# Kernel tuning notes

Measured on AMD Instinct MI355X. Metric: run time of the kernel, lower is better.

Reference implementation:

```python
import jax, jax.numpy as jnp
import numpy as np

EMB = 1024
NH = 16
HS = EMB // NH  # 64


def setup_inputs() -> dict:
    key = jax.random.key(0)
    k_x, k_wqkv, k_bqkv, k_wo, k_bo = jax.random.split(key, 5)
    x = jax.random.normal(k_x, (4, 2048, EMB), dtype=jnp.float32)
    s = 1.0 / np.sqrt(EMB)
    # torch nn.Linear weight is [out, in]; store as [in, out] for x @ W
    w_qkv = jax.random.uniform(k_wqkv, (EMB, 3 * EMB), dtype=jnp.float32, minval=-s, maxval=s)
    b_qkv = jax.random.uniform(k_bqkv, (3 * EMB,), dtype=jnp.float32, minval=-s, maxval=s)
    w_out = jax.random.uniform(k_wo, (EMB, EMB), dtype=jnp.float32, minval=-s, maxval=s)
    b_out = jax.random.uniform(k_bo, (EMB,), dtype=jnp.float32, minval=-s, maxval=s)
    return {"x": x, "w_qkv": w_qkv, "b_qkv": b_qkv, "w_out": w_out, "b_out": b_out}


def reference(x, w_qkv, b_qkv, w_out, b_out):
    B, T, C = x.shape
    qkv = x @ w_qkv + b_qkv  # [B, T, 3*C]
    q, k, v = jnp.split(qkv, 3, axis=-1)
    # [B, T, C] -> [B, nh, T, hs]
    def heads(t):
        return t.reshape(B, T, NH, HS).transpose(0, 2, 1, 3)
    q, k, v = heads(q), heads(k), heads(v)
    scores = jnp.einsum('bhqd,bhkd->bhqk', q, k) / jnp.sqrt(jnp.float32(HS))
    attn = jax.nn.softmax(scores, axis=-1)  # dropout=0 -> identity
    out = jnp.einsum('bhqk,bhkd->bhqd', attn, v)
    out = out.transpose(0, 2, 1, 3).reshape(B, T, NH * HS)
    return out @ w_out + b_out
```

## Files before the change

### kernel.cpp

```cpp
#include <hip/hip_runtime.h>

typedef unsigned short u16;
typedef unsigned int u32;
typedef __attribute__((ext_vector_type(8))) __bf16 bf16x8;
typedef __attribute__((ext_vector_type(4))) __bf16 bf16x4;
typedef __attribute__((ext_vector_type(4))) float f32x4;

#define GLD_AS1 const __attribute__((address_space(1))) void*
#define GLD_AS3 __attribute__((address_space(3))) void*

__device__ __forceinline__ u16 f2b(float f) {
  u32 u = __builtin_bit_cast(u32, f);
  u += 0x7fffu + ((u >> 16) & 1u);
  return (u16)(u >> 16);
}

__global__ void prep_kernel(const float* __restrict__ x, u16* __restrict__ xb,
                            const float* __restrict__ w_qkv, u16* __restrict__ wqkvt,
                            const float* __restrict__ w_out, u16* __restrict__ woutt) {
  __shared__ float tile[32][33];
  const int bid = blockIdx.x;
  const int tid = threadIdx.x;
  if (bid < 8192) {
    int i4 = (bid * 256 + tid) * 4;
    float4 v = *(const float4*)(x + i4);
    ushort4 o;
    o.x = f2b(v.x); o.y = f2b(v.y); o.z = f2b(v.z); o.w = f2b(v.w);
    *(ushort4*)(xb + i4) = o;
    return;
  }
  const float* src; u16* dst; int C, R, bx, by;
  if (bid < 11264) {
    int b = bid - 8192;
    src = w_qkv; dst = wqkvt; C = 3072; R = 1024;
    bx = b % 96; by = b / 96;
  } else {
    int b = bid - 11264;
    src = w_out; dst = woutt; C = 1024; R = 1024;
    bx = b % 32; by = b / 32;
  }
  const int c0 = bx * 32, r0 = by * 32;
  const int tx = tid & 31, ty = tid >> 5;
  #pragma unroll
  for (int i = ty; i < 32; i += 8)
    tile[i][tx] = src[(size_t)(r0 + i) * C + c0 + tx];
  __syncthreads();
  #pragma unroll
  for (int i = ty; i < 32; i += 8)
    dst[(size_t)(c0 + i) * R + r0 + tx] = f2b(tile[tx][i]);
}

template <int MODE>
__global__ __launch_bounds__(256)
void gemm_kernel(const u16* __restrict__ A, const u16* __restrict__ Bt,
                 const float* __restrict__ bias,
                 u16* __restrict__ qo, u16* __restrict__ ko, u16* __restrict__ vo,
                 float* __restrict__ outF, int N, int K) {
  __shared__ char As[16384];
  __shared__ char Bs[16384];
  const int tid = threadIdx.x;
  const int lane = tid & 63, wave = tid >> 6;

  const int m0 = blockIdx.x * 128, n0 = blockIdx.y * 128;
  const int wm = (wave >> 1) * 64, wn = (wave & 1) * 64;
  const int lr = lane & 15, lg = lane >> 4;

  const int rB = tid >> 3;
  const int cB = ((tid & 7) * 16) ^ ((rB & 7) << 4);

  const size_t strideK = (size_t)K * 2;
  const char* Ab = (const char*)(A + (size_t)m0 * K);
  const char* Bb = (const char*)(Bt + (size_t)n0 * K);

  f32x4 acc[4][4] = {};
  const int swr = (lr & 7) << 4;

  const int nk = K >> 6;
  for (int kt = 0; kt < nk; ++kt) {
    #pragma unroll
    for (int i = 0; i < 4; ++i)
      __builtin_amdgcn_global_load_lds(
          (GLD_AS1)(Ab + (size_t)(i * 32 + rB) * strideK + kt * 128 + cB),
          (GLD_AS3)(As + i * 4096 + tid * 16), 16, 0, 0);
    #pragma unroll
    for (int i = 0; i < 4; ++i)
      __builtin_amdgcn_global_load_lds(
          (GLD_AS1)(Bb + (size_t)(i * 32 + rB) * strideK + kt * 128 + cB),
          (GLD_AS3)(Bs + i * 4096 + tid * 16), 16, 0, 0);
    __syncthreads();

    bf16x8 af[4][2], bfr[4][2];
    #pragma unroll
    for (int m = 0; m < 4; ++m) {
      const int row = wm + m * 16 + lr;
      #pragma unroll
      for (int s = 0; s < 2; ++s)
        af[m][s] = *(const bf16x8*)(As + row * 128 + ((s * 64 + lg * 16) ^ swr));
    }
    #pragma unroll
    for (int n = 0; n < 4; ++n) {
      const int row = wn + n * 16 + lr;
      #pragma unroll
      for (int s = 0; s < 2; ++s)
        bfr[n][s] = *(const bf16x8*)(Bs + row * 128 + ((s * 64 + lg * 16) ^ swr));
    }
    __builtin_amdgcn_s_setprio(1);
    #pragma unroll
    for (int m = 0; m < 4; ++m)
      #pragma unroll
      for (int n = 0; n < 4; ++n) {
        acc[m][n] = __builtin_amdgcn_mfma_f32_16x16x32_bf16(af[m][0], bfr[n][0], acc[m][n], 0, 0, 0);
        acc[m][n] = __builtin_amdgcn_mfma_f32_16x16x32_bf16(af[m][1], bfr[n][1], acc[m][n], 0, 0, 0);
      }
    __builtin_amdgcn_s_setprio(0);
    __syncthreads();
  }

  if (MODE == 0) {
    const int b = m0 >> 11;
    #pragma unroll
    for (int n = 0; n < 4; ++n) {
      const int col = n0 + wn + n * 16 + lr;
      const float bv = bias[col];
      const int which = col >> 10, c = col & 1023;
      const int h = c >> 6, d = c & 63;
      #pragma unroll
      for (int m = 0; m < 4; ++m) {
        const int rowb = m0 + wm + m * 16 + lg * 4;
        const int t0 = rowb & 2047;
        if (which == 2) {
          const int tp = (t0 & ~31) | (8 * ((t0 >> 2) & 3) + 4 * ((t0 >> 4) & 1));
          ushort4 q4;
          q4.x = f2b(acc[m][n][0] + bv);
          q4.y = f2b(acc[m][n][1] + bv);
          q4.z = f2b(acc[m][n][2] + bv);
          q4.w = f2b(acc[m][n][3] + bv);
          *(ushort4*)&vo[((size_t)(b * 16 + h) * 64 + d) * 2048 + tp] = q4;
        } else {
          u16* dst = (which == 0) ? qo : ko;
          const float scl = (which == 0) ? 0.18033688011112042f : 1.0f;
          #pragma unroll
          for (int j = 0; j < 4; ++j) {
            float val = (acc[m][n][j] + bv) * scl;
            dst[((size_t)(b * 16 + h) * 2048 + (t0 + j)) * 64 + d] = f2b(val);
          }
        }
      }
    }
  } else {
    #pragma unroll
    for (int n = 0; n < 4; ++n) {
      const int col = n0 + wn + n * 16 + lr;
      const float bv = bias[col];
      #pragma unroll
      for (int m = 0; m < 4; ++m) {
        const int rowb = m0 + wm + m * 16 + lg * 4;
        #pragma unroll
        for (int j = 0; j < 4; ++j)
          outF[(size_t)(rowb + j) * N + col] = acc[m][n][j] + bv;
      }
    }
  }
}

__global__ __launch_bounds__(512)
void attn_kernel(const u16* __restrict__ Q, const u16* __restrict__ Kg,
                 const u16* __restrict__ Vt, u16* __restrict__ att) {
  const int tid = threadIdx.x;
  const int wave = tid >> 6, lane = tid & 63;
  const int lr = lane & 15, lg = lane >> 4;
  const int bh = blockIdx.x;
  const int q0 = blockIdx.y * 256;
  const int b = bh >> 4, h = bh & 15;

  const u16* Qh = Q + (size_t)bh * 2048 * 64;
  const char* Khb = (const char*)(Kg + (size_t)bh * 2048 * 64);
  const char* Vhb = (const char*)(Vt + (size_t)bh * 64 * 2048);

  __shared__ u16 Ks[3][64 * 64];
  __shared__ u16 Vs[3][64 * 64];

  const int rS = tid >> 3;
  const int cS = ((tid & 7) * 16) ^ ((rS & 7) << 4);

  bf16x8 qf[2][2];
  #pragma unroll
  for (int m = 0; m < 2; ++m)
    #pragma unroll
    for (int s = 0; s < 2; ++s)
      qf[m][s] = *(const bf16x8*)(Qh + (size_t)(q0 + wave * 32 + m * 16 + lr) * 64 + s * 32 + lg * 8);

  bf16x8 ones;
  #pragma unroll
  for (int e = 0; e < 8; ++e) ones[e] = (__bf16)1.0f;

  f32x4 acc[2][4] = {};
  f32x4 accl[2] = {};

#define STAGE(T, BUF)                                                          \
  {                                                                            \
    __builtin_amdgcn_global_load_lds(                                          \
        (GLD_AS1)(Khb + (size_t)((T) * 64 + rS) * 128 + cS),                   \
        (GLD_AS3)((char*)Ks[BUF] + tid * 16), 16, 0, 0);                       \
    __builtin_amdgcn_global_load_lds(                                          \
        (GLD_AS1)(Vhb + (size_t)rS * 4096 + (T) * 128 + cS),                   \
        (GLD_AS3)((char*)Vs[BUF] + tid * 16), 16, 0, 0);                       \
  }

  STAGE(0, 0);
  STAGE(1, 1);

  for (int kt = 0; kt < 32; ++kt) {
    if (kt == 31) { asm volatile("s_waitcnt vmcnt(0)" ::: "memory"); }
    else          { asm volatile("s_waitcnt vmcnt(2)" ::: "memory"); }
    __builtin_amdgcn_sched_barrier(0);
    __builtin_amdgcn_s_barrier();
    if (kt < 30) STAGE(kt + 2, (kt + 2) % 3);
    const int cur = kt % 3;

    #pragma unroll
    for (int ks = 0; ks < 2; ++ks) {
      f32x4 sf0[2] = {}, sf1[2] = {};
      __builtin_amdgcn_s_setprio(1);
      #pragma unroll
      for (int s = 0; s < 2; ++s) {
        bf16x8 kf0 = *(const bf16x8*)((const char*)Ks[cur] + (2 * ks * 16 + lr) * 128 +
                                      ((s * 64 + lg * 16) ^ ((lr & 7) << 4)));
        sf0[0] = __builtin_amdgcn_mfma_f32_16x16x32_bf16(kf0, qf[0][s], sf0[0], 0, 0, 0);
        sf0[1] = __builtin_amdgcn_mfma_f32_16x16x32_bf16(kf0, qf[1][s], sf0[1], 0, 0, 0);
        bf16x8 kf1 = *(const bf16x8*)((const char*)Ks[cur] + ((2 * ks + 1) * 16 + lr) * 128 +
                                      ((s * 64 + lg * 16) ^ ((lr & 7) << 4)));
        sf1[0] = __builtin_amdgcn_mfma_f32_16x16x32_bf16(kf1, qf[0][s], sf1[0], 0, 0, 0);
        sf1[1] = __builtin_amdgcn_mfma_f32_16x16x32_bf16(kf1, qf[1][s], sf1[1], 0, 0, 0);
      }
      __builtin_amdgcn_s_setprio(0);

      bf16x8 pa[2];
      #pragma unroll
      for (int m = 0; m < 2; ++m)
        #pragma unroll
        for (int j = 0; j < 4; ++j) {
          pa[m][j]     = (__bf16)__builtin_amdgcn_exp2f(sf0[m][j]);
          pa[m][4 + j] = (__bf16)__builtin_amdgcn_exp2f(sf1[m][j]);
        }

      __builtin_amdgcn_s_setprio(1);
      accl[0] = __builtin_amdgcn_mfma_f32_16x16x32_bf16(ones, pa[0], accl[0], 0, 0, 0);
      accl[1] = __builtin_amdgcn_mfma_f32_16x16x32_bf16(ones, pa[1], accl[1], 0, 0, 0);
      #pragma unroll
      for (int d = 0; d < 4; ++d) {
        const int rv = d * 16 + lr;
        bf16x8 vf = *(const bf16x8*)((const char*)Vs[cur] + rv * 128 +
                                     ((64 * ks + 16 * lg) ^ ((lr & 7) << 4)));
        acc[0][d] = __builtin_amdgcn_mfma_f32_16x16x32_bf16(vf, pa[0], acc[0][d], 0, 0, 0);
        acc[1][d] = __builtin_amdgcn_mfma_f32_16x16x32_bf16(vf, pa[1], acc[1][d], 0, 0, 0);
      }
      __builtin_amdgcn_s_setprio(0);
    }
  }

  #pragma unroll
  for (int m = 0; m < 2; ++m) {
    const float inv = 1.0f / accl[m][0];
    const int t = q0 + wave * 32 + m * 16 + lr;
    #pragma unroll
    for (int d = 0; d < 4; ++d) {
      bf16x4 ov;
      #pragma unroll
      for (int j = 0; j < 4; ++j) ov[j] = (__bf16)(acc[m][d][j] * inv);
      *(bf16x4*)&att[((size_t)b * 2048 + t) * 1024 + h * 64 + d * 16 + lg * 4] = ov;
    }
  }
#undef STAGE
}

extern "C" void kernel_launch(void* const* d_in, const int* in_sizes, int n_in,
                              void* d_out, int out_size, void* d_ws, size_t ws_size,
                              hipStream_t stream) {
  const float* x     = (const float*)d_in[0];
  const float* w_qkv = (const float*)d_in[1];
  const float* b_qkv = (const float*)d_in[2];
  const float* w_out = (const float*)d_in[3];
  const float* b_out = (const float*)d_in[4];
  float* out = (float*)d_out;

  char* ws = (char*)d_ws;
  const size_t MB = 1024 * 1024;
  u16* xb    = (u16*)(ws);
  u16* attb  = xb;
  u16* wqkvt = (u16*)(ws + 16 * MB);
  u16* woutt = (u16*)(ws + 22 * MB);
  u16* qb    = (u16*)(ws + 24 * MB);
  u16* kb    = (u16*)(ws + 40 * MB);
  u16* vtb   = (u16*)(ws + 56 * MB);

  prep_kernel<<<12288, 256, 0, stream>>>(x, xb, w_qkv, wqkvt, w_out, woutt);

  gemm_kernel<0><<<dim3(8192 / 128, 3072 / 128), 256, 0, stream>>>(
      xb, wqkvt, b_qkv, qb, kb, vtb, nullptr, 3072, 1024);

  attn_kernel<<<dim3(64, 8), 512, 0, stream>>>(qb, kb, vtb, attb);

  gemm_kernel<1><<<dim3(8192 / 128, 1024 / 128), 256, 0, stream>>>(
      attb, woutt, b_out, nullptr, nullptr, nullptr, out, 1024, 1024);
}
```

Baseline: 171.5 us.

## Double-buffer GEMM LDS tiles with K-step 32 to overlap loads and MFMA

```diff
diff --git a/kernel.cpp b/kernel.cpp
--- a/kernel.cpp
+++ b/kernel.cpp
@@ -56,8 +56,8 @@
                  const float* __restrict__ bias,
                  u16* __restrict__ qo, u16* __restrict__ ko, u16* __restrict__ vo,
                  float* __restrict__ outF, int N, int K) {
-  __shared__ char As[16384];
-  __shared__ char Bs[16384];
+  __shared__ char As[2][8192];
+  __shared__ char Bs[2][8192];
   const int tid = threadIdx.x;
   const int lane = tid & 63, wave = tid >> 6;
 
@@ -65,56 +65,62 @@
   const int wm = (wave >> 1) * 64, wn = (wave & 1) * 64;
   const int lr = lane & 15, lg = lane >> 4;
 
-  const int rB = tid >> 3;
-  const int cB = ((tid & 7) * 16) ^ ((rB & 7) << 4);
+  const int rS = tid >> 2;
+  const int cS = ((tid & 3) ^ (rS & 3)) << 4;
 
   const size_t strideK = (size_t)K * 2;
   const char* Ab = (const char*)(A + (size_t)m0 * K);
   const char* Bb = (const char*)(Bt + (size_t)n0 * K);
 
   f32x4 acc[4][4] = {};
-  const int swr = (lr & 7) << 4;
-
-  const int nk = K >> 6;
+
+#define GSTAGE(T, BUF)                                                         \
+  {                                                                            \
+    _Pragma("unroll")                                                          \
+    for (int i = 0; i < 2; ++i)                                                \
+      __builtin_amdgcn_global_load_lds(                                        \
+          (GLD_AS1)(Ab + (size_t)(i * 64 + rS) * strideK + (T) * 64 + cS),     \
+          (GLD_AS3)((char*)As[BUF] + i * 4096 + tid * 16), 16, 0, 0);          \
+    _Pragma("unroll")                                                          \
+    for (int i = 0; i < 2; ++i)                                                \
+      __builtin_amdgcn_global_load_lds(                                        \
+          (GLD_AS1)(Bb + (size_t)(i * 64 + rS) * strideK + (T) * 64 + cS),     \
+          (GLD_AS3)((char*)Bs[BUF] + i * 4096 + tid * 16), 16, 0, 0);          \
+  }
+
+  const int nk = K >> 5;
+  GSTAGE(0, 0);
+  asm volatile("s_waitcnt vmcnt(0)" ::: "memory");
+  __builtin_amdgcn_s_barrier();
+
   for (int kt = 0; kt < nk; ++kt) {
-    #pragma unroll
-    for (int i = 0; i < 4; ++i)
-      __builtin_amdgcn_global_load_lds(
-          (GLD_AS1)(Ab + (size_t)(i * 32 + rB) * strideK + kt * 128 + cB),
-          (GLD_AS3)(As + i * 4096 + tid * 16), 16, 0, 0);
-    #pragma unroll
-    for (int i = 0; i < 4; ++i)
-      __builtin_amdgcn_global_load_lds(
-          (GLD_AS1)(Bb + (size_t)(i * 32 + rB) * strideK + kt * 128 + cB),
-          (GLD_AS3)(Bs + i * 4096 + tid * 16), 16, 0, 0);
-    __syncthreads();
-
-    bf16x8 af[4][2], bfr[4][2];
+    const int cur = kt & 1;
+    if (kt < nk - 1) GSTAGE(kt + 1, cur ^ 1);
+
+    bf16x8 af[4], bfr[4];
     #pragma unroll
     for (int m = 0; m < 4; ++m) {
       const int row = wm + m * 16 + lr;
-      #pragma unroll
-      for (int s = 0; s < 2; ++s)
-        af[m][s] = *(const bf16x8*)(As + row * 128 + ((s * 64 + lg * 16) ^ swr));
+      af[m] = *(const bf16x8*)(As[cur] + row * 64 + ((lg ^ (lr & 3)) << 4));
     }
     #pragma unroll
     for (int n = 0; n < 4; ++n) {
       const int row = wn + n * 16 + lr;
-      #pragma unroll
-      for (int s = 0; s < 2; ++s)
-        bfr[n][s] = *(const bf16x8*)(Bs + row * 128 + ((s * 64 + lg * 16) ^ swr));
+      bfr[n] = *(const bf16x8*)(Bs[cur] + row * 64 + ((lg ^ (lr & 3)) << 4));
     }
     __builtin_amdgcn_s_setprio(1);
     #pragma unroll
     for (int m = 0; m < 4; ++m)
       #pragma unroll
-      for (int n = 0; n < 4; ++n) {
-        acc[m][n] = __builtin_amdgcn_mfma_f32_16x16x32_bf16(af[m][0], bfr[n][0], acc[m][n], 0, 0, 0);
-        acc[m][n] = __builtin_amdgcn_mfma_f32_16x16x32_bf16(af[m][1], bfr[n][1], acc[m][n], 0, 0, 0);
-      }
+      for (int n = 0; n < 4; ++n)
+        acc[m][n] = __builtin_amdgcn_mfma_f32_16x16x32_bf16(af[m], bfr[n], acc[m][n], 0, 0, 0);
     __builtin_amdgcn_s_setprio(0);
-    __syncthreads();
-  }
+
+    asm volatile("s_waitcnt vmcnt(0)" ::: "memory");
+    __builtin_amdgcn_sched_barrier(0);
+    __builtin_amdgcn_s_barrier();
+  }
+#undef GSTAGE
 
   if (MODE == 0) {
     const int b = m0 >> 11;
```

Measured after the change: 175.8 us. +2.5%, slower.
